# Performance work log

Measured on AMD Instinct MI355X. Metric: run time of the kernel, lower is better.

Reference implementation:

```python
import jax, jax.numpy as jnp
import numpy as np

B, N, H, E, M = 2, 20000, 256, 160000, 512


def setup_inputs() -> dict:
    key = jax.random.key(0)
    ks = jax.random.split(key, 8)
    s = 0.02  # small init scale like trained nets
    return {
        "h": jax.random.normal(ks[0], (B, N, H), jnp.float32),
        "edge_index": jax.random.randint(ks[1], (2, E), 0, N, jnp.int64),
        "msg_w1": jax.random.normal(ks[2], (2 * H, M), jnp.float32) * s,
        "msg_b1": jnp.zeros((M,), jnp.float32),
        "msg_w2": jax.random.normal(ks[3], (M, H), jnp.float32) * s,
        "msg_b2": jnp.zeros((H,), jnp.float32),
        "upd_w1": jax.random.normal(ks[4], (2 * H, M), jnp.float32) * s,
        "upd_b1": jnp.zeros((M,), jnp.float32),
        "upd_w2": jax.random.normal(ks[5], (M, H), jnp.float32) * s,
        "upd_b2": jnp.zeros((H,), jnp.float32),
    }


def _mlp(x, w1, b1, w2, b2):
    return jax.nn.relu(x @ w1 + b1) @ w2 + b2


def reference(h, edge_index, msg_w1, msg_b1, msg_w2, msg_b2,
              upd_w1, upd_b1, upd_w2, upd_b2):
    src, dst = edge_index[0], edge_index[1]
    h_src = h[:, src, :]                         # [B,E,H] gather
    h_dst = h[:, dst, :]                         # [B,E,H] gather
    m = _mlp(jnp.concatenate([h_src, h_dst], axis=-1),
             msg_w1, msg_b1, msg_w2, msg_b2)     # [B,E,H]
    agg = jnp.zeros_like(h).at[:, dst, :].add(m) # scatter-add over dst
    upd = _mlp(jnp.concatenate([h, agg], axis=-1),
               upd_w1, upd_b1, upd_w2, upd_b2)   # [B,N,H]
    return h + upd  # mp_residual=True
```

## Files before the change

### kernel.cpp

```cpp
#include <hip/hip_runtime.h>
#include <hip/hip_bf16.h>
#include <stdint.h>

#define B_ 2
#define N_ 20000
#define H_ 256
#define E_ 160000
#define M_ 512

typedef short bf16x8 __attribute__((ext_vector_type(8)));
typedef float f32x4 __attribute__((ext_vector_type(4)));
typedef unsigned u32x4 __attribute__((ext_vector_type(4)));

__device__ __forceinline__ unsigned short f2bf(float f) {
    union { float f; unsigned u; } cv; cv.f = f;
    unsigned u = cv.u;
    unsigned r = u + 0x7fffu + ((u >> 16) & 1u);
    return (unsigned short)(r >> 16);
}
__device__ __forceinline__ unsigned pack2(float a, float b) {
    return (unsigned)f2bf(a) | ((unsigned)f2bf(b) << 16);
}
__device__ __forceinline__ float bflo(unsigned p) {
    union { unsigned u; float f; } c; c.u = p << 16; return c.f;
}

__device__ __forceinline__ void conv_t_one(const float* __restrict__ W,
                                           unsigned short* __restrict__ Wt,
                                           int K, int Ncol, int idx) {
    int n = idx % Ncol;
    int kc = (idx / Ncol) << 3;
    unsigned short t[8];
#pragma unroll
    for (int j = 0; j < 8; ++j) t[j] = f2bf(W[(size_t)(kc + j) * Ncol + n]);
    u32x4 v;
    v.x = (unsigned)t[0] | ((unsigned)t[1] << 16);
    v.y = (unsigned)t[2] | ((unsigned)t[3] << 16);
    v.z = (unsigned)t[4] | ((unsigned)t[5] << 16);
    v.w = (unsigned)t[6] | ((unsigned)t[7] << 16);
    *(u32x4*)(Wt + (size_t)n * K + kc) = v;
}

__device__ __forceinline__ void conv_w1pq_one(const float* __restrict__ W,
                                              unsigned short* __restrict__ Wt, int idx) {
    int jj = idx & 1023;
    int kc = (idx >> 10) << 3;
    int koff = (jj >= 512) ? 256 : 0;
    int j = jj & 511;
    unsigned short t[8];
#pragma unroll
    for (int r = 0; r < 8; ++r) t[r] = f2bf(W[(size_t)(kc + r + koff) * 512 + j]);
    u32x4 v;
    v.x = (unsigned)t[0] | ((unsigned)t[1] << 16);
    v.y = (unsigned)t[2] | ((unsigned)t[3] << 16);
    v.z = (unsigned)t[4] | ((unsigned)t[5] << 16);
    v.w = (unsigned)t[6] | ((unsigned)t[7] << 16);
    *(u32x4*)(Wt + (size_t)jj * 256 + kc) = v;
}

__global__ void conv_all(const float* __restrict__ mw1, const float* __restrict__ mw2,
                         const float* __restrict__ uw1, const float* __restrict__ uw2,
                         unsigned short* __restrict__ w1pq, unsigned short* __restrict__ w2t,
                         unsigned short* __restrict__ u1t, unsigned short* __restrict__ u2t) {
    int idx = blockIdx.x * blockDim.x + threadIdx.x;
    if (idx < 32768) {
        conv_w1pq_one(mw1, w1pq, idx);
    } else if (idx < 49152) {
        conv_t_one(mw2, w2t, 512, 256, idx - 32768);
    } else if (idx < 81920) {
        conv_t_one(uw1, u1t, 512, 512, idx - 49152);
    } else if (idx < 98304) {
        conv_t_one(uw2, u2t, 512, 256, idx - 81920);
    }
}

__global__ void hist_kernel(const int* __restrict__ eidx, int* __restrict__ cnt) {
    for (int e = blockIdx.x * blockDim.x + threadIdx.x; e < E_;
         e += gridDim.x * blockDim.x)
        atomicAdd(cnt + eidx[E_ + e], 1);
}

__global__ void scan_kernel(const int* __restrict__ cnt, int* __restrict__ offs,
                            int* __restrict__ cursor) {
    __shared__ int part[1024];
    int t = threadIdx.x;
    int base_i = t * 20;
    int loc[20];
    int s = 0;
#pragma unroll 20
    for (int i = 0; i < 20; ++i) {
        int idx = base_i + i;
        int v = (idx < N_) ? cnt[idx] : 0;
        loc[i] = s;
        s += v;
    }
    part[t] = s;
    __syncthreads();
    for (int off = 1; off < 1024; off <<= 1) {
        int tmp = (t >= off) ? part[t - off] : 0;
        __syncthreads();
        if (t >= off) part[t] += tmp;
        __syncthreads();
    }
    int base = part[t] - s;
#pragma unroll 20
    for (int i = 0; i < 20; ++i) {
        int idx = base_i + i;
        if (idx < N_) {
            int o = base + loc[i];
            offs[idx] = o;
            cursor[idx] = o;
        }
    }
    if (t == 1023) offs[N_] = part[1023];
}

__global__ void scatter_kernel(const int* __restrict__ eidx, int* __restrict__ cursor,
                               int* __restrict__ srcs) {
    for (int e = blockIdx.x * blockDim.x + threadIdx.x; e < E_;
         e += gridDim.x * blockDim.x) {
        int d = eidx[E_ + e];
        int pos = atomicAdd(cursor + d, 1);
        srcs[pos] = eidx[e];
    }
}

__global__ __launch_bounds__(512, 4) void pq_gemm(
    const float* __restrict__ hb,
    const unsigned short* __restrict__ W1pq,
    unsigned short* __restrict__ PQ,
    int nrows) {
    __shared__ char smem[64 * 512];
    const int tid = threadIdx.x;
    const int tile = blockIdx.x >> 1;
    const int qh = blockIdx.x & 1;
    const int row0 = tile * 64;

#pragma unroll
    for (int it = 0; it < 8; ++it) {
        int linear = it * 512 + tid;
        int row = linear >> 6;
        int c4 = linear & 63;
        int grow = row0 + row;
        if (grow >= nrows) grow = nrows - 1;
        f32x4 v = *(const f32x4*)(hb + (size_t)grow * H_ + c4 * 4);
        int byte = (row * 512 + c4 * 8) ^ ((row & 7) << 4);
        uint2 p;
        p.x = pack2(v.x, v.y);
        p.y = pack2(v.z, v.w);
        *(uint2*)(smem + byte) = p;
    }
    __syncthreads();

    const int lane = tid & 63;
    const int w = tid >> 6;
    const int lo = lane & 15;
    const int hi = lane >> 4;
    const int colw = qh * 512 + w * 64;

    f32x4 acc[4][4];
#pragma unroll
    for (int i = 0; i < 4; ++i)
#pragma unroll
        for (int j = 0; j < 4; ++j) acc[i][j] = (f32x4){0.f, 0.f, 0.f, 0.f};

#pragma unroll
    for (int ks = 0; ks < 256; ks += 32) {
        bf16x8 af[4];
#pragma unroll
        for (int rf = 0; rf < 4; ++rf) {
            int row = rf * 16 + lo;
            int byte = (row * 512 + (ks + 8 * hi) * 2) ^ ((row & 7) << 4);
            af[rf] = *(const bf16x8*)(smem + byte);
        }
#pragma unroll
        for (int cf = 0; cf < 4; ++cf) {
            bf16x8 bfr = *(const bf16x8*)(W1pq + (size_t)(colw + cf * 16 + lo) * 256 + ks + 8 * hi);
#pragma unroll
            for (int rf = 0; rf < 4; ++rf)
                acc[rf][cf] = __builtin_amdgcn_mfma_f32_16x16x32_bf16(af[rf], bfr, acc[rf][cf], 0, 0, 0);
        }
    }

#pragma unroll
    for (int cf = 0; cf < 4; ++cf) {
        int col = colw + cf * 16 + lo;
#pragma unroll
        for (int rf = 0; rf < 4; ++rf) {
#pragma unroll
            for (int r = 0; r < 4; ++r) {
                int row = rf * 16 + hi * 4 + r;
                if (row0 + row < nrows)
                    PQ[(size_t)(row0 + row) * 1024 + col] = f2bf(acc[rf][cf][r]);
            }
        }
    }
}

__global__ __launch_bounds__(256, 8) void gather_kernel(
    const unsigned short* __restrict__ PQ,
    const int* __restrict__ srcs,
    const int* __restrict__ offs,
    const float* __restrict__ mb1,
    unsigned short* __restrict__ hsum,
    int ndst) {
    const int lane = threadIdx.x & 63;
    const int nw = (gridDim.x * blockDim.x) >> 6;
    const int wid0 = (blockIdx.x * blockDim.x + threadIdx.x) >> 6;

    float bq[8];
#pragma unroll
    for (int j = 0; j < 8; ++j) bq[j] = mb1[lane * 8 + j];

    for (int dd = wid0; dd < ndst; dd += nw) {
        int d = dd;
        size_t bofs = 0;
        if (dd >= N_) { d = dd - N_; bofs = (size_t)N_ * 1024; }
        const unsigned short* PQb = PQ + bofs;

        bf16x8 qv = *(const bf16x8*)(PQ + (size_t)dd * 1024 + 512 + lane * 8);
        float qb[8];
#pragma unroll
        for (int j = 0; j < 8; ++j)
            qb[j] = bflo((unsigned)(unsigned short)qv[j]) + bq[j];

        float acc[8];
#pragma unroll
        for (int j = 0; j < 8; ++j) acc[j] = 0.f;

        int p = offs[d];
        const int end = offs[d + 1];
        for (; p + 3 < end; p += 4) {
            int s0 = srcs[p];
            int s1 = srcs[p + 1];
            int s2 = srcs[p + 2];
            int s3 = srcs[p + 3];
            bf16x8 v0 = *(const bf16x8*)(PQb + (size_t)s0 * 1024 + lane * 8);
            bf16x8 v1 = *(const bf16x8*)(PQb + (size_t)s1 * 1024 + lane * 8);
            bf16x8 v2 = *(const bf16x8*)(PQb + (size_t)s2 * 1024 + lane * 8);
            bf16x8 v3 = *(const bf16x8*)(PQb + (size_t)s3 * 1024 + lane * 8);
#pragma unroll
            for (int j = 0; j < 8; ++j) {
                float q = qb[j];
                acc[j] += fmaxf(bflo((unsigned)(unsigned short)v0[j]) + q, 0.f)
                        + fmaxf(bflo((unsigned)(unsigned short)v1[j]) + q, 0.f)
                        + fmaxf(bflo((unsigned)(unsigned short)v2[j]) + q, 0.f)
                        + fmaxf(bflo((unsigned)(unsigned short)v3[j]) + q, 0.f);
            }
        }
        for (; p < end; ++p) {
            int s0 = srcs[p];
            bf16x8 v0 = *(const bf16x8*)(PQb + (size_t)s0 * 1024 + lane * 8);
#pragma unroll
            for (int j = 0; j < 8; ++j)
                acc[j] += fmaxf(bflo((unsigned)(unsigned short)v0[j]) + qb[j], 0.f);
        }

        u32x4 v;
        v.x = pack2(acc[0], acc[1]);
        v.y = pack2(acc[2], acc[3]);
        v.z = pack2(acc[4], acc[5]);
        v.w = pack2(acc[6], acc[7]);
        *(u32x4*)(hsum + (size_t)dd * 512 + lane * 8) = v;
    }
}

__global__ __launch_bounds__(512, 4) void mlp_kernel(
    const unsigned short* __restrict__ hsum,
    const int* __restrict__ cnt,
    const unsigned short* __restrict__ w2t,
    const float* __restrict__ mb2,
    const unsigned short* __restrict__ u1t,
    const float* __restrict__ ub1,
    const unsigned short* __restrict__ u2t,
    const float* __restrict__ ub2,
    const float* __restrict__ hb,
    float* __restrict__ outb,
    int nrows) {
    __shared__ char smA[64 * 1024];
    __shared__ int s_cnt[64];

    const int tid = threadIdx.x;
    const int d0 = blockIdx.x * 64;

    if (tid < 64) {
        int dd = d0 + tid;
        if (dd >= nrows) dd = nrows - 1;
        int node = (dd >= N_) ? dd - N_ : dd;
        s_cnt[tid] = cnt[node];
    }

#pragma unroll
    for (int it = 0; it < 8; ++it) {
        int linear = it * 512 + tid;
        int row = linear >> 6;
        int c8 = linear & 63;
        int dd = d0 + row;
        if (dd >= nrows) dd = nrows - 1;
        u32x4 v = *(const u32x4*)(hsum + (size_t)dd * 512 + c8 * 8);
        int byte = (row * 1024 + c8 * 16) ^ ((row & 7) << 4);
        *(u32x4*)(smA + byte) = v;
    }
    __syncthreads();

    const int lane = tid & 63;
    const int w = tid >> 6;
    const int lo = lane & 15;
    const int hi = lane >> 4;

    f32x4 aB[4][2];
#pragma unroll
    for (int i = 0; i < 4; ++i)
#pragma unroll
        for (int j = 0; j < 2; ++j) aB[i][j] = (f32x4){0.f, 0.f, 0.f, 0.f};
    {
        const int colw = w * 32;
#pragma unroll
        for (int ks = 0; ks < 512; ks += 32) {
            bf16x8 af[4];
#pragma unroll
            for (int rf = 0; rf < 4; ++rf) {
                int row = rf * 16 + lo;
                int byte = (row * 1024 + (ks + 8 * hi) * 2) ^ ((row & 7) << 4);
                af[rf] = *(const bf16x8*)(smA + byte);
            }
#pragma unroll
            for (int cf = 0; cf < 2; ++cf) {
                bf16x8 bfr = *(const bf16x8*)(w2t + (size_t)(colw + cf * 16 + lo) * 512 + ks + 8 * hi);
#pragma unroll
                for (int rf = 0; rf < 4; ++rf)
                    aB[rf][cf] = __builtin_amdgcn_mfma_f32_16x16x32_bf16(af[rf], bfr, aB[rf][cf], 0, 0, 0);
            }
        }
    }
    __syncthreads();

#pragma unroll
    for (int it = 0; it < 4; ++it) {
        int linear = it * 512 + tid;
        int row = linear >> 5;
        int c8 = linear & 31;
        int grow = d0 + row;
        if (grow >= nrows) grow = nrows - 1;
        const float* src = hb + (size_t)grow * H_ + c8 * 8;
        f32x4 a = *(const f32x4*)src;
        f32x4 b = *(const f32x4*)(src + 4);
        u32x4 v;
        v.x = pack2(a.x, a.y);
        v.y = pack2(a.z, a.w);
        v.z = pack2(b.x, b.y);
        v.w = pack2(b.z, b.w);
        int byte = (row * 1024 + c8 * 16) ^ ((row & 7) << 4);
        *(u32x4*)(smA + byte) = v;
    }
    {
        const int colw = w * 32;
#pragma unroll
        for (int cf = 0; cf < 2; ++cf) {
            int col = colw + cf * 16 + lo;
            float bb = mb2[col];
#pragma unroll
            for (int rf = 0; rf < 4; ++rf) {
#pragma unroll
                for (int r = 0; r < 4; ++r) {
                    int row = rf * 16 + hi * 4 + r;
                    float v = aB[rf][cf][r] + (float)s_cnt[row] * bb;
                    int byte = (row * 1024 + (256 + col) * 2) ^ ((row & 7) << 4);
                    *(unsigned short*)(smA + byte) = f2bf(v);
                }
            }
        }
    }
    __syncthreads();

    f32x4 aC[4][4];
#pragma unroll
    for (int i = 0; i < 4; ++i)
#pragma unroll
        for (int j = 0; j < 4; ++j) aC[i][j] = (f32x4){0.f, 0.f, 0.f, 0.f};
    {
        const int colw = w * 64;
#pragma unroll
        for (int ks = 0; ks < 512; ks += 32) {
            bf16x8 af[4];
#pragma unroll
            for (int rf = 0; rf < 4; ++rf) {
                int row = rf * 16 + lo;
                int byte = (row * 1024 + (ks + 8 * hi) * 2) ^ ((row & 7) << 4);
                af[rf] = *(const bf16x8*)(smA + byte);
            }
#pragma unroll
            for (int cf = 0; cf < 4; ++cf) {
                bf16x8 bfr = *(const bf16x8*)(u1t + (size_t)(colw + cf * 16 + lo) * 512 + ks + 8 * hi);
#pragma unroll
                for (int rf = 0; rf < 4; ++rf)
                    aC[rf][cf] = __builtin_amdgcn_mfma_f32_16x16x32_bf16(af[rf], bfr, aC[rf][cf], 0, 0, 0);
            }
        }
    }
    __syncthreads();

    {
        const int colw = w * 64;
#pragma unroll
        for (int cf = 0; cf < 4; ++cf) {
            int col = colw + cf * 16 + lo;
            float bb = ub1[col];
#pragma unroll
            for (int rf = 0; rf < 4; ++rf) {
#pragma unroll
                for (int r = 0; r < 4; ++r) {
                    float v = fmaxf(aC[rf][cf][r] + bb, 0.f);
                    int row = rf * 16 + hi * 4 + r;
                    int byte = (row * 1024 + col * 2) ^ ((row & 7) << 4);
                    *(unsigned short*)(smA + byte) = f2bf(v);
                }
            }
        }
    }
    __syncthreads();

    {
        const int colw = w * 32;
        f32x4 aD[4][2];
#pragma unroll
        for (int i = 0; i < 4; ++i)
#pragma unroll
            for (int j = 0; j < 2; ++j) aD[i][j] = (f32x4){0.f, 0.f, 0.f, 0.f};

#pragma unroll
        for (int ks = 0; ks < 512; ks += 32) {
            bf16x8 af[4];
#pragma unroll
            for (int rf = 0; rf < 4; ++rf) {
                int row = rf * 16 + lo;
                int byte = (row * 1024 + (ks + 8 * hi) * 2) ^ ((row & 7) << 4);
                af[rf] = *(const bf16x8*)(smA + byte);
            }
#pragma unroll
            for (int cf = 0; cf < 2; ++cf) {
                bf16x8 bfr = *(const bf16x8*)(u2t + (size_t)(colw + cf * 16 + lo) * 512 + ks + 8 * hi);
#pragma unroll
                for (int rf = 0; rf < 4; ++rf)
                    aD[rf][cf] = __builtin_amdgcn_mfma_f32_16x16x32_bf16(af[rf], bfr, aD[rf][cf], 0, 0, 0);
            }
        }

#pragma unroll
        for (int cf = 0; cf < 2; ++cf) {
            int col = colw + cf * 16 + lo;
            float bb = ub2[col];
#pragma unroll
            for (int rf = 0; rf < 4; ++rf) {
#pragma unroll
                for (int r = 0; r < 4; ++r) {
                    int row = rf * 16 + hi * 4 + r;
                    int grow = d0 + row;
                    if (grow < nrows) {
                        size_t o = (size_t)grow * H_ + col;
                        float hv = hb[o];
                        __builtin_nontemporal_store(hv + aD[rf][cf][r] + bb, &outb[o]);
                    }
                }
            }
        }
    }
}

extern "C" void kernel_launch(void* const* d_in, const int* in_sizes, int n_in,
                              void* d_out, int out_size, void* d_ws, size_t ws_size,
                              hipStream_t stream) {
    const float* h      = (const float*)d_in[0];
    const int*   eidx   = (const int*)d_in[1];
    const float* msg_w1 = (const float*)d_in[2];
    const float* msg_b1 = (const float*)d_in[3];
    const float* msg_w2 = (const float*)d_in[4];
    const float* msg_b2 = (const float*)d_in[5];
    const float* upd_w1 = (const float*)d_in[6];
    const float* upd_b1 = (const float*)d_in[7];
    const float* upd_w2 = (const float*)d_in[8];
    const float* upd_b2 = (const float*)d_in[9];
    float* out = (float*)d_out;

    const size_t smallSizes[] = {
        (size_t)2 * N_ * 1024 * 2,
        (size_t)2 * N_ * 512 * 2,
        1024 * 256 * 2,
        256 * 512 * 2,
        512 * 512 * 2,
        256 * 512 * 2,
        (size_t)N_ * 4,
        (size_t)(N_ + 1) * 4,
        (size_t)N_ * 4,
        (size_t)E_ * 4
    };
    size_t needMerged = 0;
    for (int i = 0; i < 10; ++i) needMerged += (smallSizes[i] + 255) & ~(size_t)255;
    const bool merged = (ws_size >= needMerged);

    char* ws = (char*)d_ws;
    size_t off = 0;
    auto alloc = [&](size_t bytes) {
        char* p = ws + off;
        off = (off + bytes + 255) & ~(size_t)255;
        return p;
    };
    const int PQ_ROWS = merged ? 2 * N_ : N_;
    unsigned short* PQ   = (unsigned short*)alloc((size_t)PQ_ROWS * 1024 * 2);
    unsigned short* hsum = (unsigned short*)alloc((size_t)PQ_ROWS * 512 * 2);
    unsigned short* w1pq = (unsigned short*)alloc(1024 * 256 * 2);
    unsigned short* w2t  = (unsigned short*)alloc(256 * 512 * 2);
    unsigned short* u1t  = (unsigned short*)alloc(512 * 512 * 2);
    unsigned short* u2t  = (unsigned short*)alloc(256 * 512 * 2);
    int* cnt    = (int*)alloc(N_ * 4);
    int* offs   = (int*)alloc((N_ + 1) * 4);
    int* cursor = (int*)alloc(N_ * 4);
    int* srcs   = (int*)alloc(E_ * 4);
    if (ws_size < off) return;

    hipMemsetAsync(cnt, 0, N_ * 4, stream);
    conv_all<<<384, 256, 0, stream>>>(msg_w1, msg_w2, upd_w1, upd_w2, w1pq, w2t, u1t, u2t);

    hist_kernel<<<256, 256, 0, stream>>>(eidx, cnt);
    scan_kernel<<<1, 1024, 0, stream>>>(cnt, offs, cursor);
    scatter_kernel<<<256, 256, 0, stream>>>(eidx, cursor, srcs);

    if (merged) {
        const int nrows = 2 * N_;
        const int nblk64 = (nrows + 63) / 64;
        pq_gemm<<<nblk64 * 2, 512, 0, stream>>>(h, w1pq, PQ, nrows);
        gather_kernel<<<2048, 256, 0, stream>>>(PQ, srcs, offs, msg_b1, hsum, nrows);
        const int nblkB = (N_ + 63) / 64;
        for (int b = 0; b < B_; ++b) {
            size_t ro = (size_t)b * N_;
            mlp_kernel<<<nblkB, 512, 0, stream>>>(hsum + ro * 512, cnt, w2t, msg_b2,
                                                  u1t, upd_b1, u2t, upd_b2,
                                                  h + ro * H_, out + ro * H_, N_);
        }
    } else {
        const int nblk64 = (N_ + 63) / 64;
        for (int b = 0; b < B_; ++b) {
            const float* hb = h + (size_t)b * N_ * H_;
            pq_gemm<<<nblk64 * 2, 512, 0, stream>>>(hb, w1pq, PQ, N_);
            gather_kernel<<<2048, 256, 0, stream>>>(PQ, srcs, offs, msg_b1, hsum, N_);
            mlp_kernel<<<nblk64, 512, 0, stream>>>(hsum, cnt, w2t, msg_b2,
                                                   u1t, upd_b1, u2t, upd_b2,
                                                   hb, out + (size_t)b * N_ * H_, N_);
        }
    }
}
```

Baseline: 411.0 us.

## Fold message second layer into update first layer and precompute h·U1 term

Message MLP's second-layer weight is pre-multiplied with the agg half of the update MLP's first-layer weight, with the bias folded into a per-column constant scaled by in-degree. mlp_kernel therefore runs one 512x512 GEMM on hsum instead of two chained GEMMs. The h-half of the update first layer is computed earlier by an extra pq_gemm launch into a new Rbuf buffer and added in the epilogue. The gather loop also unrolls to 8 edges, and the output store is no longer nontemporal. The trade is an extra intermediate buffer write/read and a small weight-product kernel whose fp32 product is rounded to bf16 once.

```diff
diff --git a/kernel.cpp b/kernel.cpp
--- a/kernel.cpp
+++ b/kernel.cpp
@@ -41,15 +41,22 @@
     *(u32x4*)(Wt + (size_t)n * K + kc) = v;
 }
 
-__device__ __forceinline__ void conv_w1pq_one(const float* __restrict__ W,
-                                              unsigned short* __restrict__ Wt, int idx) {
-    int jj = idx & 1023;
-    int kc = (idx >> 10) << 3;
-    int koff = (jj >= 512) ? 256 : 0;
+__device__ __forceinline__ void conv_w1pqU_one(const float* __restrict__ mw1,
+                                               const float* __restrict__ uw1,
+                                               unsigned short* __restrict__ Wt, int idx) {
+    int jj = idx % 1536;
+    int kc = (idx / 1536) << 3;
+    int seg = jj >> 9;
     int j = jj & 511;
     unsigned short t[8];
 #pragma unroll
-    for (int r = 0; r < 8; ++r) t[r] = f2bf(W[(size_t)(kc + r + koff) * 512 + j]);
+    for (int r = 0; r < 8; ++r) {
+        float x;
+        if (seg == 0)      x = mw1[(size_t)(kc + r) * 512 + j];
+        else if (seg == 1) x = mw1[(size_t)(kc + r + 256) * 512 + j];
+        else               x = uw1[(size_t)(kc + r) * 512 + j];
+        t[r] = f2bf(x);
+    }
     u32x4 v;
     v.x = (unsigned)t[0] | ((unsigned)t[1] << 16);
     v.y = (unsigned)t[2] | ((unsigned)t[3] << 16);
@@ -58,19 +65,38 @@
     *(u32x4*)(Wt + (size_t)jj * 256 + kc) = v;
 }
 
-__global__ void conv_all(const float* __restrict__ mw1, const float* __restrict__ mw2,
-                         const float* __restrict__ uw1, const float* __restrict__ uw2,
-                         unsigned short* __restrict__ w1pq, unsigned short* __restrict__ w2t,
-                         unsigned short* __restrict__ u1t, unsigned short* __restrict__ u2t) {
+__global__ void conv_all(const float* __restrict__ mw1, const float* __restrict__ uw1,
+                         const float* __restrict__ uw2,
+                         unsigned short* __restrict__ w1pqU,
+                         unsigned short* __restrict__ u2t) {
     int idx = blockIdx.x * blockDim.x + threadIdx.x;
-    if (idx < 32768) {
-        conv_w1pq_one(mw1, w1pq, idx);
-    } else if (idx < 49152) {
-        conv_t_one(mw2, w2t, 512, 256, idx - 32768);
-    } else if (idx < 81920) {
-        conv_t_one(uw1, u1t, 512, 512, idx - 49152);
-    } else if (idx < 98304) {
-        conv_t_one(uw2, u2t, 512, 256, idx - 81920);
+    if (idx < 49152) {
+        conv_w1pqU_one(mw1, uw1, w1pqU, idx);
+    } else if (idx < 65536) {
+        conv_t_one(uw2, u2t, 512, 256, idx - 49152);
+    }
+}
+
+__global__ void w12c1_kernel(const float* __restrict__ mw2, const float* __restrict__ uw1,
+                             const float* __restrict__ mb2,
+                             unsigned short* __restrict__ w12t, float* __restrict__ c1) {
+    __shared__ float u[256];
+    const int j = blockIdx.x;
+    const int t = threadIdx.x;
+    u[t] = uw1[(size_t)(256 + t) * 512 + j];
+    __syncthreads();
+#pragma unroll
+    for (int kk = 0; kk < 2; ++kk) {
+        int k = t + kk * 256;
+        const float* wrow = mw2 + (size_t)k * 256;
+        float s = 0.f;
+        for (int m = 0; m < 256; ++m) s += wrow[m] * u[m];
+        w12t[(size_t)j * 512 + k] = f2bf(s);
+    }
+    if (t == 0) {
+        float s = 0.f;
+        for (int m = 0; m < 256; ++m) s += mb2[m] * u[m];
+        c1[j] = s;
     }
 }
 
@@ -127,13 +153,13 @@
 
 __global__ __launch_bounds__(512, 4) void pq_gemm(
     const float* __restrict__ hb,
-    const unsigned short* __restrict__ W1pq,
-    unsigned short* __restrict__ PQ,
-    int nrows) {
+    const unsigned short* __restrict__ Wt,
+    unsigned short* __restrict__ outp,
+    int nrows, int qhBits, int ostride) {
     __shared__ char smem[64 * 512];
     const int tid = threadIdx.x;
-    const int tile = blockIdx.x >> 1;
-    const int qh = blockIdx.x & 1;
+    const int tile = blockIdx.x >> qhBits;
+    const int qh = blockIdx.x & ((1 << qhBits) - 1);
     const int row0 = tile * 64;
 
 #pragma unroll
@@ -175,7 +201,7 @@
         }
 #pragma unroll
         for (int cf = 0; cf < 4; ++cf) {
-            bf16x8 bfr = *(const bf16x8*)(W1pq + (size_t)(colw + cf * 16 + lo) * 256 + ks + 8 * hi);
+            bf16x8 bfr = *(const bf16x8*)(Wt + (size_t)(colw + cf * 16 + lo) * 256 + ks + 8 * hi);
 #pragma unroll
             for (int rf = 0; rf < 4; ++rf)
                 acc[rf][cf] = __builtin_amdgcn_mfma_f32_16x16x32_bf16(af[rf], bfr, acc[rf][cf], 0, 0, 0);
@@ -191,7 +217,7 @@
             for (int r = 0; r < 4; ++r) {
                 int row = rf * 16 + hi * 4 + r;
                 if (row0 + row < nrows)
-                    PQ[(size_t)(row0 + row) * 1024 + col] = f2bf(acc[rf][cf][r]);
+                    outp[(size_t)(row0 + row) * ostride + col] = f2bf(acc[rf][cf][r]);
             }
         }
     }
@@ -230,23 +256,31 @@
 
         int p = offs[d];
         const int end = offs[d + 1];
+        for (; p + 7 < end; p += 8) {
+            bf16x8 vv[8];
+#pragma unroll
+            for (int q = 0; q < 8; ++q) {
+                int sq = srcs[p + q];
+                vv[q] = *(const bf16x8*)(PQb + (size_t)sq * 1024 + lane * 8);
+            }
+#pragma unroll
+            for (int q = 0; q < 8; ++q)
+#pragma unroll
+                for (int j = 0; j < 8; ++j)
+                    acc[j] += fmaxf(bflo((unsigned)(unsigned short)vv[q][j]) + qb[j], 0.f);
+        }
         for (; p + 3 < end; p += 4) {
-            int s0 = srcs[p];
-            int s1 = srcs[p + 1];
-            int s2 = srcs[p + 2];
-            int s3 = srcs[p + 3];
-            bf16x8 v0 = *(const bf16x8*)(PQb + (size_t)s0 * 1024 + lane * 8);
-            bf16x8 v1 = *(const bf16x8*)(PQb + (size_t)s1 * 1024 + lane * 8);
-            bf16x8 v2 = *(const bf16x8*)(PQb + (size_t)s2 * 1024 + lane * 8);
-            bf16x8 v3 = *(const bf16x8*)(PQb + (size_t)s3 * 1024 + lane * 8);
-#pragma unroll
-            for (int j = 0; j < 8; ++j) {
-                float q = qb[j];
-                acc[j] += fmaxf(bflo((unsigned)(unsigned short)v0[j]) + q, 0.f)
-                        + fmaxf(bflo((unsigned)(unsigned short)v1[j]) + q, 0.f)
-                        + fmaxf(bflo((unsigned)(unsigned short)v2[j]) + q, 0.f)
-                        + fmaxf(bflo((unsigned)(unsigned short)v3[j]) + q, 0.f);
-            }
+            bf16x8 vv[4];
+#pragma unroll
+            for (int q = 0; q < 4; ++q) {
+                int sq = srcs[p + q];
+                vv[q] = *(const bf16x8*)(PQb + (size_t)sq * 1024 + lane * 8);
+            }
+#pragma unroll
+            for (int q = 0; q < 4; ++q)
+#pragma unroll
+                for (int j = 0; j < 8; ++j)
+                    acc[j] += fmaxf(bflo((unsigned)(unsigned short)vv[q][j]) + qb[j], 0.f);
         }
         for (; p < end; ++p) {
             int s0 = srcs[p];
@@ -267,10 +301,10 @@
 
 __global__ __launch_bounds__(512, 4) void mlp_kernel(
     const unsigned short* __restrict__ hsum,
+    const unsigned short* __restrict__ Rbuf,
     const int* __restrict__ cnt,
-    const unsigned short* __restrict__ w2t,
-    const float* __restrict__ mb2,
-    const unsigned short* __restrict__ u1t,
+    const unsigned short* __restrict__ w12t,
+    const float* __restrict__ c1,
     const float* __restrict__ ub1,
     const unsigned short* __restrict__ u2t,
     const float* __restrict__ ub2,
@@ -308,14 +342,13 @@
     const int lo = lane & 15;
     const int hi = lane >> 4;
 
-    f32x4 aB[4][2];
+    f32x4 aC[4][4];
 #pragma unroll
     for (int i = 0; i < 4; ++i)
 #pragma unroll
-        for (int j = 0; j < 2; ++j) aB[i][j] = (f32x4){0.f, 0.f, 0.f, 0.f};
+        for (int j = 0; j < 4; ++j) aC[i][j] = (f32x4){0.f, 0.f, 0.f, 0.f};
     {
-        const int colw = w * 32;
-#pragma unroll
+        const int colw = w * 64;
         for (int ks = 0; ks < 512; ks += 32) {
             bf16x8 af[4];
 #pragma unroll
@@ -325,93 +358,32 @@
                 af[rf] = *(const bf16x8*)(smA + byte);
             }
 #pragma unroll
-            for (int cf = 0; cf < 2; ++cf) {
-                bf16x8 bfr = *(const bf16x8*)(w2t + (size_t)(colw + cf * 16 + lo) * 512 + ks + 8 * hi);
+            for (int cf = 0; cf < 4; ++cf) {
+                bf16x8 bfr = *(const bf16x8*)(w12t + (size_t)(colw + cf * 16 + lo) * 512 + ks + 8 * hi);
 #pragma unroll
                 for (int rf = 0; rf < 4; ++rf)
-                    aB[rf][cf] = __builtin_amdgcn_mfma_f32_16x16x32_bf16(af[rf], bfr, aB[rf][cf], 0, 0, 0);
+                    aC[rf][cf] = __builtin_amdgcn_mfma_f32_16x16x32_bf16(af[rf], bfr, aC[rf][cf], 0, 0, 0);
             }
         }
     }
     __syncthreads();
 
-#pragma unroll
-    for (int it = 0; it < 4; ++it) {
-        int linear = it * 512 + tid;
-        int row = linear >> 5;
-        int c8 = linear & 31;
-        int grow = d0 + row;
-        if (grow >= nrows) grow = nrows - 1;
-        const float* src = hb + (size_t)grow * H_ + c8 * 8;
-        f32x4 a = *(const f32x4*)src;
-        f32x4 b = *(const f32x4*)(src + 4);
-        u32x4 v;
-        v.x = pack2(a.x, a.y);
-        v.y = pack2(a.z, a.w);
-        v.z = pack2(b.x, b.y);
-        v.w = pack2(b.z, b.w);
-        int byte = (row * 1024 + c8 * 16) ^ ((row & 7) << 4);
-        *(u32x4*)(smA + byte) = v;
-    }
     {
-        const int colw = w * 32;
-#pragma unroll
-        for (int cf = 0; cf < 2; ++cf) {
+        const int colw = w * 64;
+#pragma unroll
+        for (int cf = 0; cf < 4; ++cf) {
             int col = colw + cf * 16 + lo;
-            float bb = mb2[col];
+            float cb = c1[col];
+            float bb = ub1[col];
 #pragma unroll
             for (int rf = 0; rf < 4; ++rf) {
 #pragma unroll
                 for (int r = 0; r < 4; ++r) {
                     int row = rf * 16 + hi * 4 + r;
-                    float v = aB[rf][cf][r] + (float)s_cnt[row] * bb;
-                    int byte = (row * 1024 + (256 + col) * 2) ^ ((row & 7) << 4);
-                    *(unsigned short*)(smA + byte) = f2bf(v);
-                }
-            }
-        }
-    }
-    __syncthreads();
-
-    f32x4 aC[4][4];
-#pragma unroll
-    for (int i = 0; i < 4; ++i)
-#pragma unroll
-        for (int j = 0; j < 4; ++j) aC[i][j] = (f32x4){0.f, 0.f, 0.f, 0.f};
-    {
-        const int colw = w * 64;
-#pragma unroll
-        for (int ks = 0; ks < 512; ks += 32) {
-            bf16x8 af[4];
-#pragma unroll
-            for (int rf = 0; rf < 4; ++rf) {
-                int row = rf * 16 + lo;
-                int byte = (row * 1024 + (ks + 8 * hi) * 2) ^ ((row & 7) << 4);
-                af[rf] = *(const bf16x8*)(smA + byte);
-            }
-#pragma unroll
-            for (int cf = 0; cf < 4; ++cf) {
-                bf16x8 bfr = *(const bf16x8*)(u1t + (size_t)(colw + cf * 16 + lo) * 512 + ks + 8 * hi);
-#pragma unroll
-                for (int rf = 0; rf < 4; ++rf)
-                    aC[rf][cf] = __builtin_amdgcn_mfma_f32_16x16x32_bf16(af[rf], bfr, aC[rf][cf], 0, 0, 0);
-            }
-        }
-    }
-    __syncthreads();
-
-    {
-        const int colw = w * 64;
-#pragma unroll
-        for (int cf = 0; cf < 4; ++cf) {
-            int col = colw + cf * 16 + lo;
-            float bb = ub1[col];
-#pragma unroll
-            for (int rf = 0; rf < 4; ++rf) {
-#pragma unroll
-                for (int r = 0; r < 4; ++r) {
-                    float v = fmaxf(aC[rf][cf][r] + bb, 0.f);
-                    int row = rf * 16 + hi * 4 + r;
+                    int dd = d0 + row;
+                    if (dd >= nrows) dd = nrows - 1;
+                    float rv = bflo((unsigned)Rbuf[(size_t)dd * 512 + col]);
+                    float v = fmaxf(aC[rf][cf][r] + rv + (float)s_cnt[row] * cb + bb, 0.f);
                     int byte = (row * 1024 + col * 2) ^ ((row & 7) << 4);
                     *(unsigned short*)(smA + byte) = f2bf(v);
                 }
@@ -428,7 +400,6 @@
 #pragma unroll
             for (int j = 0; j < 2; ++j) aD[i][j] = (f32x4){0.f, 0.f, 0.f, 0.f};
 
-#pragma unroll
         for (int ks = 0; ks < 512; ks += 32) {
             bf16x8 af[4];
 #pragma unroll
@@ -458,8 +429,7 @@
                     int grow = d0 + row;
                     if (grow < nrows) {
                         size_t o = (size_t)grow * H_ + col;
-                        float hv = hb[o];
-                        __builtin_nontemporal_store(hv + aD[rf][cf][r] + bb, &outb[o]);
+                        outb[o] = hb[o] + aD[rf][cf][r] + bb;
                     }
                 }
             }
@@ -482,12 +452,13 @@
     const float* upd_b2 = (const float*)d_in[9];
     float* out = (float*)d_out;
 
-    const size_t smallSizes[] = {
+    const size_t mergedSizes[] = {
         (size_t)2 * N_ * 1024 * 2,
         (size_t)2 * N_ * 512 * 2,
-        1024 * 256 * 2,
-        256 * 512 * 2,
+        (size_t)2 * N_ * 512 * 2,
+        1536 * 256 * 2,
         512 * 512 * 2,
+        512 * 4,
         256 * 512 * 2,
         (size_t)N_ * 4,
         (size_t)(N_ + 1) * 4,
@@ -495,7 +466,7 @@
         (size_t)E_ * 4
     };
     size_t needMerged = 0;
-    for (int i = 0; i < 10; ++i) needMerged += (smallSizes[i] + 255) & ~(size_t)255;
+    for (int i = 0; i < 11; ++i) needMerged += (mergedSizes[i] + 255) & ~(size_t)255;
     const bool merged = (ws_size >= needMerged);
 
     char* ws = (char*)d_ws;
@@ -505,13 +476,14 @@
         off = (off + bytes + 255) & ~(size_t)255;
         return p;
     };
-    const int PQ_ROWS = merged ? 2 * N_ : N_;
-    unsigned short* PQ   = (unsigned short*)alloc((size_t)PQ_ROWS * 1024 * 2);
-    unsigned short* hsum = (unsigned short*)alloc((size_t)PQ_ROWS * 512 * 2);
-    unsigned short* w1pq = (unsigned short*)alloc(1024 * 256 * 2);
-    unsigned short* w2t  = (unsigned short*)alloc(256 * 512 * 2);
-    unsigned short* u1t  = (unsigned short*)alloc(512 * 512 * 2);
-    unsigned short* u2t  = (unsigned short*)alloc(256 * 512 * 2);
+    const int RWS = merged ? 2 * N_ : N_;
+    unsigned short* PQ    = (unsigned short*)alloc((size_t)RWS * 1024 * 2);
+    unsigned short* hsum  = (unsigned short*)alloc((size_t)RWS * 512 * 2);
+    unsigned short* Rbuf  = (unsigned short*)alloc((size_t)RWS * 512 * 2);
+    unsigned short* w1pqU = (unsigned short*)alloc(1536 * 256 * 2);
+    unsigned short* w12t  = (unsigned short*)alloc(512 * 512 * 2);
+    float*          c1    = (float*)alloc(512 * 4);
+    unsigned short* u2t   = (unsigned short*)alloc(256 * 512 * 2);
     int* cnt    = (int*)alloc(N_ * 4);
     int* offs   = (int*)alloc((N_ + 1) * 4);
     int* cursor = (int*)alloc(N_ * 4);
@@ -519,33 +491,38 @@
     if (ws_size < off) return;
 
     hipMemsetAsync(cnt, 0, N_ * 4, stream);
-    conv_all<<<384, 256, 0, stream>>>(msg_w1, msg_w2, upd_w1, upd_w2, w1pq, w2t, u1t, u2t);
+    conv_all<<<256, 256, 0, stream>>>(msg_w1, upd_w1, upd_w2, w1pqU, u2t);
+    w12c1_kernel<<<512, 256, 0, stream>>>(msg_w2, upd_w1, msg_b2, w12t, c1);
 
     hist_kernel<<<256, 256, 0, stream>>>(eidx, cnt);
     scan_kernel<<<1, 1024, 0, stream>>>(cnt, offs, cursor);
     scatter_kernel<<<256, 256, 0, stream>>>(eidx, cursor, srcs);
 
+    const unsigned short* wR = w1pqU + (size_t)1024 * 256;
+
     if (merged) {
         const int nrows = 2 * N_;
-        const int nblk64 = (nrows + 63) / 64;
-        pq_gemm<<<nblk64 * 2, 512, 0, stream>>>(h, w1pq, PQ, nrows);
+        const int nblk = (nrows + 63) / 64;
+        pq_gemm<<<nblk * 2, 512, 0, stream>>>(h, w1pqU, PQ, nrows, 1, 1024);
+        pq_gemm<<<nblk, 512, 0, stream>>>(h, wR, Rbuf, nrows, 0, 512);
         gather_kernel<<<2048, 256, 0, stream>>>(PQ, srcs, offs, msg_b1, hsum, nrows);
         const int nblkB = (N_ + 63) / 64;
         for (int b = 0; b < B_; ++b) {
             size_t ro = (size_t)b * N_;
-            mlp_kernel<<<nblkB, 512, 0, stream>>>(hsum + ro * 512, cnt, w2t, msg_b2,
-                                                  u1t, upd_b1, u2t, upd_b2,
+            mlp_kernel<<<nblkB, 512, 0, stream>>>(hsum + ro * 512, Rbuf + ro * 512, cnt,
+                                                  w12t, c1, upd_b1, u2t, upd_b2,
                                                   h + ro * H_, out + ro * H_, N_);
         }
     } else {
-        const int nblk64 = (N_ + 63) / 64;
+        const int nblk = (N_ + 63) / 64;
         for (int b = 0; b < B_; ++b) {
             const float* hb = h + (size_t)b * N_ * H_;
-            pq_gemm<<<nblk64 * 2, 512, 0, stream>>>(hb, w1pq, PQ, N_);
+            pq_gemm<<<nblk * 2, 512, 0, stream>>>(hb, w1pqU, PQ, N_, 1, 1024);
+            pq_gemm<<<nblk, 512, 0, stream>>>(hb, wR, Rbuf, N_, 0, 512);
             gather_kernel<<<2048, 256, 0, stream>>>(PQ, srcs, offs, msg_b1, hsum, N_);
-            mlp_kernel<<<nblk64, 512, 0, stream>>>(hsum, cnt, w2t, msg_b2,
-                                                   u1t, upd_b1, u2t, upd_b2,
-                                                   hb, out + (size_t)b * N_ * H_, N_);
-        }
-    }
-}
+            mlp_kernel<<<nblk, 512, 0, stream>>>(hsum, Rbuf, cnt,
+                                                 w12t, c1, upd_b1, u2t, upd_b2,
+                                                 hb, out + (size_t)b * N_ * H_, N_);
+        }
+    }
+}
```

Measured after the change: 547.8 us. 1.33x slower.

## Gather source projections in FP8 and drop merged-batch path

Applied to the files above, without the earlier changes.

Adds a kernel that converts the source half of the per-node projection (P) from bf16 to fp8, and has the gather read 8 bytes per lane instead of 16. This halves the traffic of the random gathers. It also removes the merged two-batch path so batches always run one at a time, adding an extra launch per batch. It further removes full unrolling of the MLP k-loops and the nontemporal output stores. FP8 lowers the precision of the message pre-activations, and the per-batch launches and conversion pass add overhead.

```diff
diff --git a/kernel.cpp b/kernel.cpp
--- a/kernel.cpp
+++ b/kernel.cpp
@@ -10,7 +10,9 @@
 
 typedef short bf16x8 __attribute__((ext_vector_type(8)));
 typedef float f32x4 __attribute__((ext_vector_type(4)));
+typedef float f32x2 __attribute__((ext_vector_type(2)));
 typedef unsigned u32x4 __attribute__((ext_vector_type(4)));
+typedef unsigned u32x2 __attribute__((ext_vector_type(2)));
 
 __device__ __forceinline__ unsigned short f2bf(float f) {
     union { float f; unsigned u; } cv; cv.f = f;
@@ -23,6 +25,21 @@
 }
 __device__ __forceinline__ float bflo(unsigned p) {
     union { unsigned u; float f; } c; c.u = p << 16; return c.f;
+}
+
+__device__ __forceinline__ void acc_fp8(u32x2 vv, const float* qb, float* acc) {
+    f32x2 a0 = __builtin_amdgcn_cvt_pk_f32_fp8(vv.x, false);
+    f32x2 a1 = __builtin_amdgcn_cvt_pk_f32_fp8(vv.x, true);
+    f32x2 a2 = __builtin_amdgcn_cvt_pk_f32_fp8(vv.y, false);
+    f32x2 a3 = __builtin_amdgcn_cvt_pk_f32_fp8(vv.y, true);
+    acc[0] += fmaxf(a0.x + qb[0], 0.f);
+    acc[1] += fmaxf(a0.y + qb[1], 0.f);
+    acc[2] += fmaxf(a1.x + qb[2], 0.f);
+    acc[3] += fmaxf(a1.y + qb[3], 0.f);
+    acc[4] += fmaxf(a2.x + qb[4], 0.f);
+    acc[5] += fmaxf(a2.y + qb[5], 0.f);
+    acc[6] += fmaxf(a3.x + qb[6], 0.f);
+    acc[7] += fmaxf(a3.y + qb[7], 0.f);
 }
 
 __device__ __forceinline__ void conv_t_one(const float* __restrict__ W,
@@ -197,7 +214,31 @@
     }
 }
 
+__global__ void p8_kernel(const unsigned short* __restrict__ PQ,
+                          unsigned char* __restrict__ Pf8, int nrows) {
+    int total = nrows * 64;
+    for (int idx = blockIdx.x * blockDim.x + threadIdx.x; idx < total;
+         idx += gridDim.x * blockDim.x) {
+        int row = idx >> 6;
+        int c8 = idx & 63;
+        bf16x8 v = *(const bf16x8*)(PQ + (size_t)row * 1024 + c8 * 8);
+        float f[8];
+#pragma unroll
+        for (int j = 0; j < 8; ++j) f[j] = bflo((unsigned)(unsigned short)v[j]);
+        unsigned lo = 0, hi = 0;
+        lo = __builtin_amdgcn_cvt_pk_fp8_f32(f[0], f[1], lo, false);
+        lo = __builtin_amdgcn_cvt_pk_fp8_f32(f[2], f[3], lo, true);
+        hi = __builtin_amdgcn_cvt_pk_fp8_f32(f[4], f[5], hi, false);
+        hi = __builtin_amdgcn_cvt_pk_fp8_f32(f[6], f[7], hi, true);
+        u32x2 o;
+        o.x = lo;
+        o.y = hi;
+        *(u32x2*)(Pf8 + (size_t)row * 512 + c8 * 8) = o;
+    }
+}
+
 __global__ __launch_bounds__(256, 8) void gather_kernel(
+    const unsigned char* __restrict__ Pf8,
     const unsigned short* __restrict__ PQ,
     const int* __restrict__ srcs,
     const int* __restrict__ offs,
@@ -213,11 +254,6 @@
     for (int j = 0; j < 8; ++j) bq[j] = mb1[lane * 8 + j];
 
     for (int dd = wid0; dd < ndst; dd += nw) {
-        int d = dd;
-        size_t bofs = 0;
-        if (dd >= N_) { d = dd - N_; bofs = (size_t)N_ * 1024; }
-        const unsigned short* PQb = PQ + bofs;
-
         bf16x8 qv = *(const bf16x8*)(PQ + (size_t)dd * 1024 + 512 + lane * 8);
         float qb[8];
 #pragma unroll
@@ -228,32 +264,26 @@
 #pragma unroll
         for (int j = 0; j < 8; ++j) acc[j] = 0.f;
 
-        int p = offs[d];
-        const int end = offs[d + 1];
+        int p = offs[dd];
+        const int end = offs[dd + 1];
         for (; p + 3 < end; p += 4) {
             int s0 = srcs[p];
             int s1 = srcs[p + 1];
             int s2 = srcs[p + 2];
             int s3 = srcs[p + 3];
-            bf16x8 v0 = *(const bf16x8*)(PQb + (size_t)s0 * 1024 + lane * 8);
-            bf16x8 v1 = *(const bf16x8*)(PQb + (size_t)s1 * 1024 + lane * 8);
-            bf16x8 v2 = *(const bf16x8*)(PQb + (size_t)s2 * 1024 + lane * 8);
-            bf16x8 v3 = *(const bf16x8*)(PQb + (size_t)s3 * 1024 + lane * 8);
-#pragma unroll
-            for (int j = 0; j < 8; ++j) {
-                float q = qb[j];
-                acc[j] += fmaxf(bflo((unsigned)(unsigned short)v0[j]) + q, 0.f)
-                        + fmaxf(bflo((unsigned)(unsigned short)v1[j]) + q, 0.f)
-                        + fmaxf(bflo((unsigned)(unsigned short)v2[j]) + q, 0.f)
-                        + fmaxf(bflo((unsigned)(unsigned short)v3[j]) + q, 0.f);
-            }
+            u32x2 v0 = *(const u32x2*)(Pf8 + (size_t)s0 * 512 + lane * 8);
+            u32x2 v1 = *(const u32x2*)(Pf8 + (size_t)s1 * 512 + lane * 8);
+            u32x2 v2 = *(const u32x2*)(Pf8 + (size_t)s2 * 512 + lane * 8);
+            u32x2 v3 = *(const u32x2*)(Pf8 + (size_t)s3 * 512 + lane * 8);
+            acc_fp8(v0, qb, acc);
+            acc_fp8(v1, qb, acc);
+            acc_fp8(v2, qb, acc);
+            acc_fp8(v3, qb, acc);
         }
         for (; p < end; ++p) {
             int s0 = srcs[p];
-            bf16x8 v0 = *(const bf16x8*)(PQb + (size_t)s0 * 1024 + lane * 8);
-#pragma unroll
-            for (int j = 0; j < 8; ++j)
-                acc[j] += fmaxf(bflo((unsigned)(unsigned short)v0[j]) + qb[j], 0.f);
+            u32x2 v0 = *(const u32x2*)(Pf8 + (size_t)s0 * 512 + lane * 8);
+            acc_fp8(v0, qb, acc);
         }
 
         u32x4 v;
@@ -286,8 +316,7 @@
     if (tid < 64) {
         int dd = d0 + tid;
         if (dd >= nrows) dd = nrows - 1;
-        int node = (dd >= N_) ? dd - N_ : dd;
-        s_cnt[tid] = cnt[node];
+        s_cnt[tid] = cnt[dd];
     }
 
 #pragma unroll
@@ -315,7 +344,6 @@
         for (int j = 0; j < 2; ++j) aB[i][j] = (f32x4){0.f, 0.f, 0.f, 0.f};
     {
         const int colw = w * 32;
-#pragma unroll
         for (int ks = 0; ks < 512; ks += 32) {
             bf16x8 af[4];
 #pragma unroll
@@ -380,7 +408,6 @@
         for (int j = 0; j < 4; ++j) aC[i][j] = (f32x4){0.f, 0.f, 0.f, 0.f};
     {
         const int colw = w * 64;
-#pragma unroll
         for (int ks = 0; ks < 512; ks += 32) {
             bf16x8 af[4];
 #pragma unroll
@@ -428,7 +455,6 @@
 #pragma unroll
             for (int j = 0; j < 2; ++j) aD[i][j] = (f32x4){0.f, 0.f, 0.f, 0.f};
 
-#pragma unroll
         for (int ks = 0; ks < 512; ks += 32) {
             bf16x8 af[4];
 #pragma unroll
@@ -458,8 +484,7 @@
                     int grow = d0 + row;
                     if (grow < nrows) {
                         size_t o = (size_t)grow * H_ + col;
-                        float hv = hb[o];
-                        __builtin_nontemporal_store(hv + aD[rf][cf][r] + bb, &outb[o]);
+                        outb[o] = hb[o] + aD[rf][cf][r] + bb;
                     }
                 }
             }
@@ -482,22 +507,6 @@
     const float* upd_b2 = (const float*)d_in[9];
     float* out = (float*)d_out;
 
-    const size_t smallSizes[] = {
-        (size_t)2 * N_ * 1024 * 2,
-        (size_t)2 * N_ * 512 * 2,
-        1024 * 256 * 2,
-        256 * 512 * 2,
-        512 * 512 * 2,
-        256 * 512 * 2,
-        (size_t)N_ * 4,
-        (size_t)(N_ + 1) * 4,
-        (size_t)N_ * 4,
-        (size_t)E_ * 4
-    };
-    size_t needMerged = 0;
-    for (int i = 0; i < 10; ++i) needMerged += (smallSizes[i] + 255) & ~(size_t)255;
-    const bool merged = (ws_size >= needMerged);
-
     char* ws = (char*)d_ws;
     size_t off = 0;
     auto alloc = [&](size_t bytes) {
@@ -505,9 +514,9 @@
         off = (off + bytes + 255) & ~(size_t)255;
         return p;
     };
-    const int PQ_ROWS = merged ? 2 * N_ : N_;
-    unsigned short* PQ   = (unsigned short*)alloc((size_t)PQ_ROWS * 1024 * 2);
-    unsigned short* hsum = (unsigned short*)alloc((size_t)PQ_ROWS * 512 * 2);
+    unsigned short* PQ   = (unsigned short*)alloc((size_t)N_ * 1024 * 2);
+    unsigned char*  Pf8  = (unsigned char*)alloc((size_t)N_ * 512);
+    unsigned short* hsum = (unsigned short*)alloc((size_t)N_ * 512 * 2);
     unsigned short* w1pq = (unsigned short*)alloc(1024 * 256 * 2);
     unsigned short* w2t  = (unsigned short*)alloc(256 * 512 * 2);
     unsigned short* u1t  = (unsigned short*)alloc(512 * 512 * 2);
@@ -525,27 +534,14 @@
     scan_kernel<<<1, 1024, 0, stream>>>(cnt, offs, cursor);
     scatter_kernel<<<256, 256, 0, stream>>>(eidx, cursor, srcs);
 
-    if (merged) {
-        const int nrows = 2 * N_;
-        const int nblk64 = (nrows + 63) / 64;
-        pq_gemm<<<nblk64 * 2, 512, 0, stream>>>(h, w1pq, PQ, nrows);
-        gather_kernel<<<2048, 256, 0, stream>>>(PQ, srcs, offs, msg_b1, hsum, nrows);
-        const int nblkB = (N_ + 63) / 64;
-        for (int b = 0; b < B_; ++b) {
-            size_t ro = (size_t)b * N_;
-            mlp_kernel<<<nblkB, 512, 0, stream>>>(hsum + ro * 512, cnt, w2t, msg_b2,
-                                                  u1t, upd_b1, u2t, upd_b2,
-                                                  h + ro * H_, out + ro * H_, N_);
-        }
-    } else {
-        const int nblk64 = (N_ + 63) / 64;
-        for (int b = 0; b < B_; ++b) {
-            const float* hb = h + (size_t)b * N_ * H_;
-            pq_gemm<<<nblk64 * 2, 512, 0, stream>>>(hb, w1pq, PQ, N_);
-            gather_kernel<<<2048, 256, 0, stream>>>(PQ, srcs, offs, msg_b1, hsum, N_);
-            mlp_kernel<<<nblk64, 512, 0, stream>>>(hsum, cnt, w2t, msg_b2,
-                                                   u1t, upd_b1, u2t, upd_b2,
-                                                   hb, out + (size_t)b * N_ * H_, N_);
-        }
-    }
-}
+    const int nblk = (N_ + 63) / 64;
+    for (int b = 0; b < B_; ++b) {
+        const float* hb = h + (size_t)b * N_ * H_;
+        pq_gemm<<<nblk * 2, 512, 0, stream>>>(hb, w1pq, PQ, N_);
+        p8_kernel<<<1280, 256, 0, stream>>>(PQ, Pf8, N_);
+        gather_kernel<<<2048, 256, 0, stream>>>(Pf8, PQ, srcs, offs, msg_b1, hsum, N_);
+        mlp_kernel<<<nblk, 512, 0, stream>>>(hsum, cnt, w2t, msg_b2,
+                                             u1t, upd_b1, u2t, upd_b2,
+                                             hb, out + (size_t)b * N_ * H_, N_);
+    }
+}
```

Result: no change. 414.3 us (+0.8%).
